# Kernel optimization log

Hardware: AMD Instinct MI355X
Metric: run time of the kernel (lower is better)

The kernel has to match this reference:

```python
import jax, jax.numpy as jnp
import numpy as np

N = 8192
EPS = 1e-12

def setup_inputs() -> dict:
    key = jax.random.key(0)
    k1, k2 = jax.random.split(key)
    var_1 = jax.random.normal(k1, (N,), dtype=jnp.float32)          # e.g. bb mass
    var_2 = jax.random.uniform(k2, (N,), dtype=jnp.float32)          # classifier output in (0,1)
    normedweight = jnp.ones((N,), dtype=jnp.float32)                 # weights sum to N
    return {"var_1": var_1, "var_2": var_2, "normedweight": normedweight, "power": 2}


def reference(var_1, var_2, normedweight, power):
    # Pairwise absolute difference matrices [N, N]
    amat = jnp.abs(var_1[:, None] - var_1[None, :])
    bmat = jnp.abs(var_2[:, None] - var_2[None, :])

    # Weighted row means (weight broadcasts along columns, mean over axis=1)
    amatavg = jnp.mean(amat * normedweight, axis=1)                  # [N]
    bmatavg = jnp.mean(bmat * normedweight, axis=1)                  # [N]

    # Double centering: minuend_1[i,j] = avg[j], minuend_2[i,j] = avg[i]
    Amat = amat - amatavg[None, :] - amatavg[:, None] + jnp.mean(amatavg * normedweight)
    Bmat = bmat - bmatavg[None, :] - bmatavg[:, None] + jnp.mean(bmatavg * normedweight)

    ABavg = jnp.abs(jnp.mean(Amat * Bmat * normedweight, axis=1))    # [N]
    AAavg = jnp.mean(Amat * Amat * normedweight, axis=1)             # [N]
    BBavg = jnp.mean(Bmat * Bmat * normedweight, axis=1)             # [N]

    num = jnp.mean(ABavg * normedweight)
    den = jnp.abs(jnp.mean(AAavg * normedweight) * jnp.mean(BBavg * normedweight))

    if power == 1:
        dCorr = num / jnp.sqrt(den + EPS)
    elif power == 2:
        dCorr = num ** 2 / (den + EPS)
    else:
        dCorr = (num / jnp.sqrt(jnp.mean(AAavg * normedweight) * jnp.mean(BBavg * normedweight)) + EPS) ** power

    # Original clamps NaN and negative results to 0
    dCorr = jnp.where(jnp.isnan(dCorr), jnp.float32(0.0), dCorr)
    dCorr = jnp.maximum(dCorr, jnp.float32(0.0))
    return dCorr
```

## Files before the change

### kernel.cpp

```cpp
#include <hip/hip_runtime.h>
#include <math.h>


#define NN 8192
#define BLK 256
#define RPT 4
#define ROWS_PER_BLOCK 16
#define GRIDX 512
#define CSPLIT 4
#define SEGC 2048
#define ITERS 8
#define NBLK (GRIDX * CSPLIT)
#define MIDB 32
#define INV_N (1.0f / NN)
#define NSC 9

__device__ __forceinline__ void p1_elem(
    float aj, float bj, float wj,
    const float* __restrict__ ai, const float* __restrict__ bi,
    float* __restrict__ sa, float* __restrict__ sb) {
#pragma unroll
  for (int m = 0; m < RPT; ++m) {
    sa[m] = fmaf(fabsf(ai[m] - aj), wj, sa[m]);
    sb[m] = fmaf(fabsf(bi[m] - bj), wj, sb[m]);
  }
}

__global__ __launch_bounds__(BLK) void k_pass1(
    const float* __restrict__ a, const float* __restrict__ b,
    const float* __restrict__ w,
    float* __restrict__ pa, float* __restrict__ pb,
    double* __restrict__ gpa, double* __restrict__ gpb) {
  const int lane = threadIdx.x & 63;
  const int wv = threadIdx.x >> 6;
  const int i0 = blockIdx.x * ROWS_PER_BLOCK + wv * RPT;
  const int seg = blockIdx.y;

  float ai[RPT], bi[RPT], sa[RPT], sb[RPT];
#pragma unroll
  for (int m = 0; m < RPT; ++m) {
    ai[m] = a[i0 + m]; bi[m] = b[i0 + m];
    sa[m] = 0.f; sb[m] = 0.f;
  }

  const int jb = seg * SEGC;
  const float4* a4 = (const float4*)(a + jb) + lane;
  const float4* b4 = (const float4*)(b + jb) + lane;
  const float4* w4 = (const float4*)(w + jb) + lane;

  float4 A0 = a4[0], B0 = b4[0], W0 = w4[0];
#pragma unroll 1
  for (int k = 0; k < ITERS - 1; ++k) {
    const int nx = (k + 1) * 64;
    const float4 A1 = a4[nx], B1 = b4[nx], W1 = w4[nx];
    p1_elem(A0.x, B0.x, W0.x, ai, bi, sa, sb);
    p1_elem(A0.y, B0.y, W0.y, ai, bi, sa, sb);
    p1_elem(A0.z, B0.z, W0.z, ai, bi, sa, sb);
    p1_elem(A0.w, B0.w, W0.w, ai, bi, sa, sb);
    A0 = A1; B0 = B1; W0 = W1;
  }
  p1_elem(A0.x, B0.x, W0.x, ai, bi, sa, sb);
  p1_elem(A0.y, B0.y, W0.y, ai, bi, sa, sb);
  p1_elem(A0.z, B0.z, W0.z, ai, bi, sa, sb);
  p1_elem(A0.w, B0.w, W0.w, ai, bi, sa, sb);

#pragma unroll
  for (int off = 32; off >= 1; off >>= 1) {
#pragma unroll
    for (int m = 0; m < RPT; ++m) {
      sa[m] += __shfl_xor(sa[m], off);
      sb[m] += __shfl_xor(sb[m], off);
    }
  }

  __shared__ double gla[4], glb[4];
  if (lane == 0) {
#pragma unroll
    for (int m = 0; m < RPT; ++m) {
      pa[seg * NN + i0 + m] = sa[m];
      pb[seg * NN + i0 + m] = sb[m];
    }
    double da = 0.0, db = 0.0;
#pragma unroll
    for (int m = 0; m < RPT; ++m) {
      const double wi = (double)w[i0 + m];
      da += (double)sa[m] * wi;
      db += (double)sb[m] * wi;
    }
    gla[wv] = da; glb[wv] = db;
  }
  __syncthreads();
  if (threadIdx.x == 0) {
    const int bid = blockIdx.y * GRIDX + blockIdx.x;
    gpa[bid] = gla[0] + gla[1] + gla[2] + gla[3];
    gpb[bid] = glb[0] + glb[1] + glb[2] + glb[3];
  }
}

__global__ __launch_bounds__(BLK) void k_mid(
    const float* __restrict__ a, const float* __restrict__ b,
    const float* __restrict__ w,
    const float* __restrict__ pa, const float* __restrict__ pb,
    const double* __restrict__ gpa, const double* __restrict__ gpb,
    float* __restrict__ rr, float* __restrict__ ss,
    double* __restrict__ scal, double* __restrict__ hs) {
  const int lane = threadIdx.x & 63;
  const int wv = threadIdx.x >> 6;

  __shared__ double gsum[2];
  if (wv < 2) {
    const double* g = wv ? gpb : gpa;
    double s = 0.0;
    for (int k = 0; k < NBLK / 64; ++k) s += g[lane + 64 * k];
#pragma unroll
    for (int off = 32; off >= 1; off >>= 1) s += __shfl_xor(s, off);
    if (lane == 0) gsum[wv] = s;
  }
  __syncthreads();
  const double n2 = (double)NN * (double)NN;
  const float ha = (float)(0.5 * gsum[0] / n2);
  const float hb = (float)(0.5 * gsum[1] / n2);
  if (blockIdx.x == 0 && threadIdx.x == 0) { hs[0] = (double)ha; hs[1] = (double)hb; }

  const int i = blockIdx.x * BLK + threadIdx.x;
  const float av = (pa[i] + pa[NN + i] + pa[2 * NN + i] + pa[3 * NN + i]) * INV_N;
  const float bv = (pb[i] + pb[NN + i] + pb[2 * NN + i] + pb[3 * NN + i]) * INV_N;
  const float ri = av - ha;
  const float si = bv - hb;
  const float wi = w[i], aiv = a[i], biv = b[i];
  rr[i] = ri;  ss[i] = si;

  double p[NSC];
  p[0] = (double)wi;
  p[1] = (double)wi * aiv;
  p[2] = (double)wi * aiv * aiv;
  p[3] = (double)wi * biv;
  p[4] = (double)wi * biv * biv;
  p[5] = (double)wi * ri;
  p[6] = (double)wi * si;
  p[7] = (double)wi * ri * ri;
  p[8] = (double)wi * si * si;
#pragma unroll
  for (int off = 32; off >= 1; off >>= 1) {
#pragma unroll
    for (int t = 0; t < NSC; ++t) p[t] += __shfl_xor(p[t], off);
  }
  __shared__ double lp[NSC][4];
  if (lane == 0) {
#pragma unroll
    for (int t = 0; t < NSC; ++t) lp[t][wv] = p[t];
  }
  __syncthreads();
  if (threadIdx.x == 0) {
#pragma unroll
    for (int t = 0; t < NSC; ++t)
      scal[t * MIDB + blockIdx.x] = lp[t][0] + lp[t][1] + lp[t][2] + lp[t][3];
  }
}

__global__ __launch_bounds__(BLK) void k_pass2(
    const float* __restrict__ a, const float* __restrict__ b,
    const float* __restrict__ w,
    const float* __restrict__ rr, const float* __restrict__ ss,
    float* __restrict__ Qp) {
  const int lane = threadIdx.x & 63;
  const int wv = threadIdx.x >> 6;
  const int i0 = blockIdx.x * ROWS_PER_BLOCK + wv * RPT;
  const int seg = blockIdx.y;

  float ai[RPT], bi[RPT], q[RPT];
#pragma unroll
  for (int m = 0; m < RPT; ++m) {
    ai[m] = a[i0 + m]; bi[m] = b[i0 + m];
    q[m] = 0.f;
  }

  const int jb = seg * SEGC;
  const float4* a4 = (const float4*)(a + jb)  + lane;
  const float4* b4 = (const float4*)(b + jb)  + lane;
  const float4* w4 = (const float4*)(w + jb)  + lane;
  const float4* r4 = (const float4*)(rr + jb) + lane;
  const float4* s4 = (const float4*)(ss + jb) + lane;

#pragma unroll 1
  for (int k = 0; k < ITERS; ++k) {
    const int ix = k * 64;
    const float4 A = a4[ix], B = b4[ix], Wt = w4[ix], R = r4[ix], S = s4[ix];
#define P2E(e)                                            \
    {                                                     \
      _Pragma("unroll")                                   \
      for (int m = 0; m < RPT; ++m) {                     \
        const float dp = fabsf(ai[m] - A.e) - R.e;        \
        const float ep = fabsf(bi[m] - B.e) - S.e;        \
        q[m] = fmaf(Wt.e * dp, ep, q[m]);                 \
      }                                                   \
    }
    P2E(x) P2E(y) P2E(z) P2E(w)
#undef P2E
  }

#pragma unroll
  for (int off = 32; off >= 1; off >>= 1) {
#pragma unroll
    for (int m = 0; m < RPT; ++m) q[m] += __shfl_xor(q[m], off);
  }
  if (lane == 0) {
#pragma unroll
    for (int m = 0; m < RPT; ++m) Qp[seg * NN + i0 + m] = q[m];
  }
}

__global__ __launch_bounds__(BLK) void k_tail(
    const float* __restrict__ w,
    const float* __restrict__ rr, const float* __restrict__ ss,
    const float* __restrict__ Qp,
    const double* __restrict__ scal, const double* __restrict__ hs,
    double* __restrict__ fAB) {
  const int lane = threadIdx.x & 63;
  const int wv = threadIdx.x >> 6;

  __shared__ double sc3[3];
  if (threadIdx.x < 3) {
    const int t = (threadIdx.x == 0) ? 0 : (threadIdx.x == 1) ? 5 : 6;
    double s = 0.0;
    for (int k = 0; k < MIDB; ++k) s += scal[t * MIDB + k];
    sc3[threadIdx.x] = s;
  }
  __syncthreads();
  const double W = sc3[0], Swr = sc3[1], Sws = sc3[2];
  const double ha = hs[0], hb = hs[1];

  const int i = blockIdx.x * BLK + threadIdx.x;
  const double Qi = (double)Qp[i] + Qp[NN + i] + Qp[2 * NN + i] + Qp[3 * NN + i];
  const double ri = (double)rr[i];
  const double si = (double)ss[i];
  const double wi = (double)w[i];
  const double P0a = ((double)rr[i] + ha) * (double)NN;
  const double P0b = ((double)ss[i] + hb) * (double)NN;

  const double TAB = Qi - si * (P0a - Swr) - ri * (P0b - Sws) + ri * si * W;

  double ab = fabs(TAB) * wi;
#pragma unroll
  for (int off = 32; off >= 1; off >>= 1) ab += __shfl_xor(ab, off);
  __shared__ double l[4];
  if (lane == 0) l[wv] = ab;
  __syncthreads();
  if (threadIdx.x == 0) fAB[blockIdx.x] = l[0] + l[1] + l[2] + l[3];
}

__global__ __launch_bounds__(64) void k_fin(
    const double* __restrict__ fAB, const double* __restrict__ scal,
    const double* __restrict__ hs, const int* __restrict__ powerPtr,
    float* __restrict__ out) {
  const int lane = threadIdx.x;

  double ab = (lane < MIDB) ? fAB[lane] : 0.0;
#pragma unroll
  for (int off = 32; off >= 1; off >>= 1) ab += __shfl_xor(ab, off);

  __shared__ double sc[NSC];
  if (lane < NSC) {
    double s = 0.0;
    for (int k = 0; k < MIDB; ++k) s += scal[lane * MIDB + k];
    sc[lane] = s;
  }
  __syncthreads();

  if (lane == 0) {
    const double n2 = (double)NN * (double)NN;
    const double W = sc[0], Ma1 = sc[1], Ma2 = sc[2], Mb1 = sc[3], Mb2 = sc[4];
    const double Swr = sc[5], Sws = sc[6], Swr2 = sc[7], Sws2 = sc[8];
    const double ha = hs[0], hb = hs[1];

    const double S_AA = 2.0 * W * Ma2 - 2.0 * Ma1 * Ma1
                      - 4.0 * (double)NN * (Swr2 + ha * Swr)
                      + 2.0 * W * Swr2 + 2.0 * Swr * Swr;
    const double S_BB = 2.0 * W * Mb2 - 2.0 * Mb1 * Mb1
                      - 4.0 * (double)NN * (Sws2 + hb * Sws)
                      + 2.0 * W * Sws2 + 2.0 * Sws * Sws;

    const double num = ab / n2;
    const double mAA = S_AA / n2;
    const double mBB = S_BB / n2;
    const double den = fabs(mAA * mBB);
    const int p = powerPtr[0];
    double d;
    if (p == 1) {
      d = num / sqrt(den + 1e-12);
    } else if (p == 2) {
      d = (num * num) / (den + 1e-12);
    } else {
      d = pow(num / sqrt(mAA * mBB) + 1e-12, (double)p);
    }
    if (isnan(d)) d = 0.0;
    if (d < 0.0) d = 0.0;
    out[0] = (float)d;
  }
}

extern "C" void kernel_launch(void* const* d_in, const int* in_sizes, int n_in,
                              void* d_out, int out_size, void* d_ws, size_t ws_size,
                              hipStream_t stream) {
  const float* a = (const float*)d_in[0];
  const float* b = (const float*)d_in[1];
  const float* w = (const float*)d_in[2];
  const int* power = (const int*)d_in[3];
  float* out = (float*)d_out;

  double* dws = (double*)d_ws;
  double* gpa  = dws;
  double* gpb  = gpa + NBLK;
  double* scal = gpb + NBLK;
  double* hs   = scal + NSC * MIDB;
  double* fAB  = hs + 2;
  float* fp    = (float*)(fAB + MIDB);
  float* pa    = fp;
  float* pb    = pa + 4 * NN;
  float* Qp    = pb + 4 * NN;
  float* rr    = Qp + 4 * NN;
  float* ss    = rr + NN;

  const dim3 grid(GRIDX, CSPLIT);
  k_pass1<<<grid, BLK, 0, stream>>>(a, b, w, pa, pb, gpa, gpb);
  k_mid<<<MIDB, BLK, 0, stream>>>(a, b, w, pa, pb, gpa, gpb, rr, ss, scal, hs);
  k_pass2<<<grid, BLK, 0, stream>>>(a, b, w, rr, ss, Qp);
  k_tail<<<MIDB, BLK, 0, stream>>>(w, rr, ss, Qp, scal, hs, fAB);
  k_fin<<<1, 64, 0, stream>>>(fAB, scal, hs, power, out);
}
```

Baseline: 40.15 us.

## Fuse tail and final kernels into one single-block kernel, move scalar sums there

```diff
diff --git a/kernel.cpp b/kernel.cpp
--- a/kernel.cpp
+++ b/kernel.cpp
@@ -12,6 +12,7 @@
 #define ITERS 8
 #define NBLK (GRIDX * CSPLIT)
 #define MIDB 32
+#define BLKF 1024
 #define INV_N (1.0f / NN)
 #define NSC 9
 
@@ -98,12 +99,11 @@
 }
 
 __global__ __launch_bounds__(BLK) void k_mid(
-    const float* __restrict__ a, const float* __restrict__ b,
     const float* __restrict__ w,
     const float* __restrict__ pa, const float* __restrict__ pb,
     const double* __restrict__ gpa, const double* __restrict__ gpb,
     float* __restrict__ rr, float* __restrict__ ss,
-    double* __restrict__ scal, double* __restrict__ hs) {
+    double* __restrict__ hs) {
   const int lane = threadIdx.x & 63;
   const int wv = threadIdx.x >> 6;
 
@@ -125,37 +125,8 @@
   const int i = blockIdx.x * BLK + threadIdx.x;
   const float av = (pa[i] + pa[NN + i] + pa[2 * NN + i] + pa[3 * NN + i]) * INV_N;
   const float bv = (pb[i] + pb[NN + i] + pb[2 * NN + i] + pb[3 * NN + i]) * INV_N;
-  const float ri = av - ha;
-  const float si = bv - hb;
-  const float wi = w[i], aiv = a[i], biv = b[i];
-  rr[i] = ri;  ss[i] = si;
-
-  double p[NSC];
-  p[0] = (double)wi;
-  p[1] = (double)wi * aiv;
-  p[2] = (double)wi * aiv * aiv;
-  p[3] = (double)wi * biv;
-  p[4] = (double)wi * biv * biv;
-  p[5] = (double)wi * ri;
-  p[6] = (double)wi * si;
-  p[7] = (double)wi * ri * ri;
-  p[8] = (double)wi * si * si;
-#pragma unroll
-  for (int off = 32; off >= 1; off >>= 1) {
-#pragma unroll
-    for (int t = 0; t < NSC; ++t) p[t] += __shfl_xor(p[t], off);
-  }
-  __shared__ double lp[NSC][4];
-  if (lane == 0) {
-#pragma unroll
-    for (int t = 0; t < NSC; ++t) lp[t][wv] = p[t];
-  }
-  __syncthreads();
-  if (threadIdx.x == 0) {
-#pragma unroll
-    for (int t = 0; t < NSC; ++t)
-      scal[t * MIDB + blockIdx.x] = lp[t][0] + lp[t][1] + lp[t][2] + lp[t][3];
-  }
+  rr[i] = av - ha;
+  ss[i] = bv - hb;
 }
 
 __global__ __launch_bounds__(BLK) void k_pass2(
@@ -210,68 +181,78 @@
   }
 }
 
-__global__ __launch_bounds__(BLK) void k_tail(
+__global__ __launch_bounds__(BLKF) void k_tailfin(
+    const float* __restrict__ a, const float* __restrict__ b,
     const float* __restrict__ w,
     const float* __restrict__ rr, const float* __restrict__ ss,
-    const float* __restrict__ Qp,
-    const double* __restrict__ scal, const double* __restrict__ hs,
-    double* __restrict__ fAB) {
+    const float* __restrict__ Qp, const double* __restrict__ hs,
+    const int* __restrict__ powerPtr, float* __restrict__ out) {
   const int lane = threadIdx.x & 63;
-  const int wv = threadIdx.x >> 6;
-
-  __shared__ double sc3[3];
-  if (threadIdx.x < 3) {
-    const int t = (threadIdx.x == 0) ? 0 : (threadIdx.x == 1) ? 5 : 6;
+  const int wvf = threadIdx.x >> 6;
+  const double n2 = (double)NN * (double)NN;
+  const double ha = hs[0], hb = hs[1];
+
+  double p[NSC];
+#pragma unroll
+  for (int t = 0; t < NSC; ++t) p[t] = 0.0;
+  for (int k = 0; k < NN / BLKF; ++k) {
+    const int i = threadIdx.x + k * BLKF;
+    const double wi = (double)w[i];
+    const double aiv = (double)a[i], biv = (double)b[i];
+    const double ri = (double)rr[i], si = (double)ss[i];
+    p[0] += wi;
+    p[1] += wi * aiv;
+    p[2] += wi * aiv * aiv;
+    p[3] += wi * biv;
+    p[4] += wi * biv * biv;
+    p[5] += wi * ri;
+    p[6] += wi * si;
+    p[7] += wi * ri * ri;
+    p[8] += wi * si * si;
+  }
+#pragma unroll
+  for (int off = 32; off >= 1; off >>= 1) {
+#pragma unroll
+    for (int t = 0; t < NSC; ++t) p[t] += __shfl_xor(p[t], off);
+  }
+  __shared__ double lp[NSC][16];
+  __shared__ double sc[NSC];
+  if (lane == 0) {
+#pragma unroll
+    for (int t = 0; t < NSC; ++t) lp[t][wvf] = p[t];
+  }
+  __syncthreads();
+  if (threadIdx.x < NSC) {
     double s = 0.0;
-    for (int k = 0; k < MIDB; ++k) s += scal[t * MIDB + k];
-    sc3[threadIdx.x] = s;
-  }
-  __syncthreads();
-  const double W = sc3[0], Swr = sc3[1], Sws = sc3[2];
-  const double ha = hs[0], hb = hs[1];
-
-  const int i = blockIdx.x * BLK + threadIdx.x;
-  const double Qi = (double)Qp[i] + Qp[NN + i] + Qp[2 * NN + i] + Qp[3 * NN + i];
-  const double ri = (double)rr[i];
-  const double si = (double)ss[i];
-  const double wi = (double)w[i];
-  const double P0a = ((double)rr[i] + ha) * (double)NN;
-  const double P0b = ((double)ss[i] + hb) * (double)NN;
-
-  const double TAB = Qi - si * (P0a - Swr) - ri * (P0b - Sws) + ri * si * W;
-
-  double ab = fabs(TAB) * wi;
+    for (int t = 0; t < 16; ++t) s += lp[threadIdx.x][t];
+    sc[threadIdx.x] = s;
+  }
+  __syncthreads();
+  const double W = sc[0], Swr = sc[5], Sws = sc[6];
+
+  double ab = 0.0;
+  for (int k = 0; k < NN / BLKF; ++k) {
+    const int i = threadIdx.x + k * BLKF;
+    const double Qi = (double)Qp[i] + Qp[NN + i] + Qp[2 * NN + i] + Qp[3 * NN + i];
+    const double ri = (double)rr[i];
+    const double si = (double)ss[i];
+    const double wi = (double)w[i];
+    const double P0a = (ri + ha) * (double)NN;
+    const double P0b = (si + hb) * (double)NN;
+    const double TAB = Qi - si * (P0a - Swr) - ri * (P0b - Sws) + ri * si * W;
+    ab += fabs(TAB) * wi;
+  }
 #pragma unroll
   for (int off = 32; off >= 1; off >>= 1) ab += __shfl_xor(ab, off);
-  __shared__ double l[4];
-  if (lane == 0) l[wv] = ab;
-  __syncthreads();
-  if (threadIdx.x == 0) fAB[blockIdx.x] = l[0] + l[1] + l[2] + l[3];
-}
-
-__global__ __launch_bounds__(64) void k_fin(
-    const double* __restrict__ fAB, const double* __restrict__ scal,
-    const double* __restrict__ hs, const int* __restrict__ powerPtr,
-    float* __restrict__ out) {
-  const int lane = threadIdx.x;
-
-  double ab = (lane < MIDB) ? fAB[lane] : 0.0;
-#pragma unroll
-  for (int off = 32; off >= 1; off >>= 1) ab += __shfl_xor(ab, off);
-
-  __shared__ double sc[NSC];
-  if (lane < NSC) {
-    double s = 0.0;
-    for (int k = 0; k < MIDB; ++k) s += scal[lane * MIDB + k];
-    sc[lane] = s;
-  }
-  __syncthreads();
-
-  if (lane == 0) {
-    const double n2 = (double)NN * (double)NN;
-    const double W = sc[0], Ma1 = sc[1], Ma2 = sc[2], Mb1 = sc[3], Mb2 = sc[4];
-    const double Swr = sc[5], Sws = sc[6], Swr2 = sc[7], Sws2 = sc[8];
-    const double ha = hs[0], hb = hs[1];
+  __shared__ double l[16];
+  if (lane == 0) l[wvf] = ab;
+  __syncthreads();
+
+  if (threadIdx.x == 0) {
+    double sab = 0.0;
+    for (int t = 0; t < 16; ++t) sab += l[t];
+    const double Ma1 = sc[1], Ma2 = sc[2], Mb1 = sc[3], Mb2 = sc[4];
+    const double Swr2 = sc[7], Sws2 = sc[8];
 
     const double S_AA = 2.0 * W * Ma2 - 2.0 * Ma1 * Ma1
                       - 4.0 * (double)NN * (Swr2 + ha * Swr)
@@ -280,18 +261,18 @@
                       - 4.0 * (double)NN * (Sws2 + hb * Sws)
                       + 2.0 * W * Sws2 + 2.0 * Sws * Sws;
 
-    const double num = ab / n2;
+    const double num = sab / n2;
     const double mAA = S_AA / n2;
     const double mBB = S_BB / n2;
     const double den = fabs(mAA * mBB);
-    const int p = powerPtr[0];
+    const int pw = powerPtr[0];
     double d;
-    if (p == 1) {
+    if (pw == 1) {
       d = num / sqrt(den + 1e-12);
-    } else if (p == 2) {
+    } else if (pw == 2) {
       d = (num * num) / (den + 1e-12);
     } else {
-      d = pow(num / sqrt(mAA * mBB) + 1e-12, (double)p);
+      d = pow(num / sqrt(mAA * mBB) + 1e-12, (double)pw);
     }
     if (isnan(d)) d = 0.0;
     if (d < 0.0) d = 0.0;
@@ -309,22 +290,19 @@
   float* out = (float*)d_out;
 
   double* dws = (double*)d_ws;
-  double* gpa  = dws;
-  double* gpb  = gpa + NBLK;
-  double* scal = gpb + NBLK;
-  double* hs   = scal + NSC * MIDB;
-  double* fAB  = hs + 2;
-  float* fp    = (float*)(fAB + MIDB);
-  float* pa    = fp;
-  float* pb    = pa + 4 * NN;
-  float* Qp    = pb + 4 * NN;
-  float* rr    = Qp + 4 * NN;
-  float* ss    = rr + NN;
+  double* gpa = dws;
+  double* gpb = gpa + NBLK;
+  double* hs  = gpb + NBLK;
+  float* fp   = (float*)(hs + 2);
+  float* pa   = fp;
+  float* pb   = pa + 4 * NN;
+  float* Qp   = pb + 4 * NN;
+  float* rr   = Qp + 4 * NN;
+  float* ss   = rr + NN;
 
   const dim3 grid(GRIDX, CSPLIT);
   k_pass1<<<grid, BLK, 0, stream>>>(a, b, w, pa, pb, gpa, gpb);
-  k_mid<<<MIDB, BLK, 0, stream>>>(a, b, w, pa, pb, gpa, gpb, rr, ss, scal, hs);
+  k_mid<<<MIDB, BLK, 0, stream>>>(w, pa, pb, gpa, gpb, rr, ss, hs);
   k_pass2<<<grid, BLK, 0, stream>>>(a, b, w, rr, ss, Qp);
-  k_tail<<<MIDB, BLK, 0, stream>>>(w, rr, ss, Qp, scal, hs, fAB);
-  k_fin<<<1, 64, 0, stream>>>(fAB, scal, hs, power, out);
-}
+  k_tailfin<<<1, BLKF, 0, stream>>>(a, b, w, rr, ss, Qp, hs, power, out);
+}
```

After: 43.12 us. 1.07x slower.

## Fuse tail reduction into pass2 by splitting columns across waves in-block

Applied to the files above, without the earlier changes.

```diff
diff --git a/kernel.cpp b/kernel.cpp
--- a/kernel.cpp
+++ b/kernel.cpp
@@ -12,6 +12,7 @@
 #define ITERS 8
 #define NBLK (GRIDX * CSPLIT)
 #define MIDB 32
+#define G2BLK 2048
 #define INV_N (1.0f / NN)
 #define NSC 9
 
@@ -162,11 +163,21 @@
     const float* __restrict__ a, const float* __restrict__ b,
     const float* __restrict__ w,
     const float* __restrict__ rr, const float* __restrict__ ss,
-    float* __restrict__ Qp) {
+    const double* __restrict__ scal, const double* __restrict__ hs,
+    double* __restrict__ fAB) {
   const int lane = threadIdx.x & 63;
   const int wv = threadIdx.x >> 6;
-  const int i0 = blockIdx.x * ROWS_PER_BLOCK + wv * RPT;
-  const int seg = blockIdx.y;
+  const int i0 = blockIdx.x * RPT;
+
+  double Wd   = scal[0 * MIDB + (lane & 31)];
+  double Swrd = scal[5 * MIDB + (lane & 31)];
+  double Swsd = scal[6 * MIDB + (lane & 31)];
+#pragma unroll
+  for (int off = 16; off >= 1; off >>= 1) {
+    Wd   += __shfl_xor(Wd, off);
+    Swrd += __shfl_xor(Swrd, off);
+    Swsd += __shfl_xor(Swsd, off);
+  }
 
   float ai[RPT], bi[RPT], q[RPT];
 #pragma unroll
@@ -175,7 +186,7 @@
     q[m] = 0.f;
   }
 
-  const int jb = seg * SEGC;
+  const int jb = wv * SEGC;
   const float4* a4 = (const float4*)(a + jb)  + lane;
   const float4* b4 = (const float4*)(b + jb)  + lane;
   const float4* w4 = (const float4*)(w + jb)  + lane;
@@ -204,71 +215,56 @@
 #pragma unroll
     for (int m = 0; m < RPT; ++m) q[m] += __shfl_xor(q[m], off);
   }
+
+  __shared__ float lq[CSPLIT][RPT];
+  __shared__ double lab[RPT];
   if (lane == 0) {
 #pragma unroll
-    for (int m = 0; m < RPT; ++m) Qp[seg * NN + i0 + m] = q[m];
-  }
-}
-
-__global__ __launch_bounds__(BLK) void k_tail(
-    const float* __restrict__ w,
-    const float* __restrict__ rr, const float* __restrict__ ss,
-    const float* __restrict__ Qp,
-    const double* __restrict__ scal, const double* __restrict__ hs,
-    double* __restrict__ fAB) {
-  const int lane = threadIdx.x & 63;
-  const int wv = threadIdx.x >> 6;
-
-  __shared__ double sc3[3];
-  if (threadIdx.x < 3) {
-    const int t = (threadIdx.x == 0) ? 0 : (threadIdx.x == 1) ? 5 : 6;
-    double s = 0.0;
-    for (int k = 0; k < MIDB; ++k) s += scal[t * MIDB + k];
-    sc3[threadIdx.x] = s;
-  }
-  __syncthreads();
-  const double W = sc3[0], Swr = sc3[1], Sws = sc3[2];
-  const double ha = hs[0], hb = hs[1];
-
-  const int i = blockIdx.x * BLK + threadIdx.x;
-  const double Qi = (double)Qp[i] + Qp[NN + i] + Qp[2 * NN + i] + Qp[3 * NN + i];
-  const double ri = (double)rr[i];
-  const double si = (double)ss[i];
-  const double wi = (double)w[i];
-  const double P0a = ((double)rr[i] + ha) * (double)NN;
-  const double P0b = ((double)ss[i] + hb) * (double)NN;
-
-  const double TAB = Qi - si * (P0a - Swr) - ri * (P0b - Sws) + ri * si * W;
-
-  double ab = fabs(TAB) * wi;
-#pragma unroll
-  for (int off = 32; off >= 1; off >>= 1) ab += __shfl_xor(ab, off);
-  __shared__ double l[4];
-  if (lane == 0) l[wv] = ab;
-  __syncthreads();
-  if (threadIdx.x == 0) fAB[blockIdx.x] = l[0] + l[1] + l[2] + l[3];
-}
-
-__global__ __launch_bounds__(64) void k_fin(
+    for (int m = 0; m < RPT; ++m) lq[wv][m] = q[m];
+  }
+  __syncthreads();
+  if (threadIdx.x < RPT) {
+    const int m = threadIdx.x;
+    const double Qi = (double)lq[0][m] + lq[1][m] + lq[2][m] + lq[3][m];
+    const double ha = hs[0], hb = hs[1];
+    const double ri = (double)rr[i0 + m];
+    const double si = (double)ss[i0 + m];
+    const double wi = (double)w[i0 + m];
+    const double P0a = (ri + ha) * (double)NN;
+    const double P0b = (si + hb) * (double)NN;
+    const double TAB = Qi - si * (P0a - Swrd) - ri * (P0b - Swsd) + ri * si * Wd;
+    lab[m] = fabs(TAB) * wi;
+  }
+  __syncthreads();
+  if (threadIdx.x == 0)
+    fAB[blockIdx.x] = lab[0] + lab[1] + lab[2] + lab[3];
+}
+
+__global__ __launch_bounds__(BLK) void k_fin(
     const double* __restrict__ fAB, const double* __restrict__ scal,
     const double* __restrict__ hs, const int* __restrict__ powerPtr,
     float* __restrict__ out) {
-  const int lane = threadIdx.x;
-
-  double ab = (lane < MIDB) ? fAB[lane] : 0.0;
+  const int lane = threadIdx.x & 63;
+  const int wv = threadIdx.x >> 6;
+
+  double ab = 0.0;
+#pragma unroll
+  for (int k = 0; k < G2BLK / BLK; ++k) ab += fAB[threadIdx.x + k * BLK];
 #pragma unroll
   for (int off = 32; off >= 1; off >>= 1) ab += __shfl_xor(ab, off);
-
+  __shared__ double l[4];
   __shared__ double sc[NSC];
-  if (lane < NSC) {
+  if (lane == 0) l[wv] = ab;
+  if (threadIdx.x < NSC) {
     double s = 0.0;
-    for (int k = 0; k < MIDB; ++k) s += scal[lane * MIDB + k];
-    sc[lane] = s;
-  }
-  __syncthreads();
-
-  if (lane == 0) {
+    for (int k = 0; k < MIDB; ++k) s += scal[threadIdx.x * MIDB + k];
+    sc[threadIdx.x] = s;
+  }
+  __syncthreads();
+
+  if (threadIdx.x == 0) {
     const double n2 = (double)NN * (double)NN;
+    const double sab = l[0] + l[1] + l[2] + l[3];
     const double W = sc[0], Ma1 = sc[1], Ma2 = sc[2], Mb1 = sc[3], Mb2 = sc[4];
     const double Swr = sc[5], Sws = sc[6], Swr2 = sc[7], Sws2 = sc[8];
     const double ha = hs[0], hb = hs[1];
@@ -280,7 +276,7 @@
                       - 4.0 * (double)NN * (Sws2 + hb * Sws)
                       + 2.0 * W * Sws2 + 2.0 * Sws * Sws;
 
-    const double num = ab / n2;
+    const double num = sab / n2;
     const double mAA = S_AA / n2;
     const double mBB = S_BB / n2;
     const double den = fabs(mAA * mBB);
@@ -314,17 +310,15 @@
   double* scal = gpb + NBLK;
   double* hs   = scal + NSC * MIDB;
   double* fAB  = hs + 2;
-  float* fp    = (float*)(fAB + MIDB);
+  float* fp    = (float*)(fAB + G2BLK);
   float* pa    = fp;
   float* pb    = pa + 4 * NN;
-  float* Qp    = pb + 4 * NN;
-  float* rr    = Qp + 4 * NN;
+  float* rr    = pb + 4 * NN;
   float* ss    = rr + NN;
 
   const dim3 grid(GRIDX, CSPLIT);
   k_pass1<<<grid, BLK, 0, stream>>>(a, b, w, pa, pb, gpa, gpb);
   k_mid<<<MIDB, BLK, 0, stream>>>(a, b, w, pa, pb, gpa, gpb, rr, ss, scal, hs);
-  k_pass2<<<grid, BLK, 0, stream>>>(a, b, w, rr, ss, Qp);
-  k_tail<<<MIDB, BLK, 0, stream>>>(w, rr, ss, Qp, scal, hs, fAB);
-  k_fin<<<1, 64, 0, stream>>>(fAB, scal, hs, power, out);
-}
+  k_pass2<<<G2BLK, BLK, 0, stream>>>(a, b, w, rr, ss, scal, hs, fAB);
+  k_fin<<<1, BLK, 0, stream>>>(fAB, scal, hs, power, out);
+}
```

New measurement: 39.48 us. About the same (-1.7%).
